# Kernel optimization log

Measured on AMD Instinct MI355X. Metric: run time of the kernel, lower is better.

The kernel has to match this reference:

```python
import jax, jax.numpy as jnp
import numpy as np

P, M, N, H, B, E, K = 50, 512, 1024, 256, 8, 400, 5
ALPHA_MAX, TAU_MAX, RHO_MAX, ETA_MAX = 0.01, 1.0, 1.0, 1.0
LEAK = 0.01  # F.leaky_relu default slope


def _lrelu(x):
    return jnp.where(x >= 0, x, LEAK * x)


def _layernorm(x, g, b, eps=1e-5):
    mu = jnp.mean(x, axis=-1, keepdims=True)
    var = jnp.mean((x - mu) ** 2, axis=-1, keepdims=True)
    return (x - mu) * jax.lax.rsqrt(var + eps) * g + b


def setup_inputs() -> dict:
    ks = iter(jax.random.split(jax.random.key(0), 16))

    def w(fin, fout):
        return jax.random.normal(next(ks), (fin, fout), jnp.float32) * np.float32(np.sqrt(2.0 / (fin + fout)))

    H4 = 4 * H
    inp = {
        'A': jax.random.normal(next(ks), (1, P, M, N), jnp.float32) * 0.05,
        'b': jax.random.normal(next(ks), (B, P, M, 1), jnp.float32),
        'W1': w(2 * N, H), 'b1': jnp.zeros(H), 'bn1_s': jnp.ones(H), 'bn1_t': jnp.zeros(H),
        'W2': w(H, 2 * H), 'b2': jnp.zeros(2 * H), 'bn2_s': jnp.ones(2 * H), 'bn2_t': jnp.zeros(2 * H),
        'W3': w(2 * H, H4), 'b3': jnp.zeros(H4), 'bn3_s': jnp.ones(H4), 'bn3_t': jnp.zeros(H4),
        'W4': w(H4, H4), 'b4': jnp.zeros(H4), 'bn4_s': jnp.ones(H4), 'bn4_t': jnp.zeros(H4),
        'W5': w(H4, H4), 'b5': jnp.zeros(H4), 'bn5_s': jnp.ones(H4), 'bn5_t': jnp.zeros(H4),
        'ln_g': jnp.ones(H4), 'ln_b': jnp.zeros(H4),
        'Wd1': w(P * H4, H4), 'bd1': jnp.zeros(H4), 'lnd1_g': jnp.ones(H4), 'lnd1_b': jnp.zeros(H4),
        'Wd2': w(H4, 2 * H), 'bd2': jnp.zeros(2 * H), 'lnd2_g': jnp.ones(2 * H), 'lnd2_b': jnp.zeros(2 * H),
        'Wd3': w(2 * H, H), 'bd3': jnp.zeros(H), 'lnd3_g': jnp.ones(H), 'lnd3_b': jnp.zeros(H),
        'Wfc': w(H, 4) * 0.1, 'bfc': jnp.zeros(4),
        'edge_index': jax.random.randint(next(ks), (2, E), 0, P),
    }
    return inp


def reference(A, b, W1, b1, bn1_s, bn1_t, W2, b2, bn2_s, bn2_t, W3, b3, bn3_s, bn3_t,
              W4, b4, bn4_s, bn4_t, W5, b5, bn5_s, bn5_t, ln_g, ln_b,
              Wd1, bd1, lnd1_g, lnd1_b, Wd2, bd2, lnd2_g, lnd2_b, Wd3, bd3, lnd3_g, lnd3_b,
              Wfc, bfc, edge_index):
    A0 = A[0]                                             # [P,M,N]
    AtA = jnp.einsum('pmi,pmj->pij', A0, A0)              # [P,N,N]  (compute_Atx(A))
    Atb = jnp.einsum('pmn,bpm->bpn', A0, b[..., 0])[..., None]  # [B,P,N,1]

    src, dst = edge_index[0], edge_index[1]
    ones_e = jnp.ones((E,), A.dtype)
    # sum_neighbors: out-degree of each node p, shape broadcastable to [B,P,1,1]
    sum_nb = jax.ops.segment_sum(ones_e, src, num_segments=P)[None, :, None, None]

    # GCNConv normalization with self loops: norm_ij = deg_i^-1/2 * deg_j^-1/2
    sl = jnp.arange(P)
    src_a = jnp.concatenate([src, sl])
    dst_a = jnp.concatenate([dst, sl])
    deg = jax.ops.segment_sum(jnp.ones((E + P,), A.dtype), dst_a, num_segments=P)
    dinv = jax.lax.rsqrt(deg)
    coef = (dinv[src_a] * dinv[dst_a])[:, None]           # [E+P,1]

    convs = [(W1, b1, bn1_s, bn1_t), (W2, b2, bn2_s, bn2_t), (W3, b3, bn3_s, bn3_t),
             (W4, b4, bn4_s, bn4_t), (W5, b5, bn5_s, bn5_t)]

    def gconv(x, W, bias):                                # x: [P,Cin]
        xw = x @ W
        return jax.ops.segment_sum(xw[src_a] * coef, dst_a, num_segments=P) + bias

    def encode_one(feat):                                 # feat: [P,2N]
        x = feat
        for (W, bias, s, t) in convs:
            # leaky_relu -> BatchNorm1d (eval: affine scale/shift) -> dropout (eval: id)
            x = _lrelu(gconv(x, W, bias)) * s + t
        return _layernorm(x, ln_g, ln_b).reshape(-1)      # [P*4H]

    enc = jax.vmap(encode_one)

    y = jnp.zeros((B, P, N, 1), A.dtype)
    U = jnp.zeros_like(y)
    delta = jnp.zeros_like(y)
    Ys = []
    for k in range(K):
        AtAy = jnp.einsum('pij,bpj->bpi', AtA, y[..., 0])[..., None]  # [B,P,N,1]
        feat = jnp.concatenate([AtAy, Atb], axis=2)[..., 0]           # [B,P,2N]
        code = enc(feat)                                              # [B,P*4H]
        h = _lrelu(_layernorm(code @ Wd1 + bd1, lnd1_g, lnd1_b))
        h = _lrelu(_layernorm(h @ Wd2 + bd2, lnd2_g, lnd2_b))
        h = _lrelu(_layernorm(h @ Wd3 + bd3, lnd3_g, lnd3_b))
        hyp = jnp.clip(jax.nn.sigmoid(h @ Wfc + bfc), 1e-4, 0.99).reshape(B, 4, 1, 1, 1)
        alpha = hyp[:, 0] * ALPHA_MAX
        tau = hyp[:, 1] * TAU_MAX
        rho = hyp[:, 2] * RHO_MAX
        eta = hyp[:, 3] * ETA_MAX
        g = AtAy - Atb + jnp.sign(y) * tau + U * sum_nb + delta * rho
        mg = max(30.0, 100.0 - k)
        g = jnp.clip(g, -mg, mg)
        mv = max(10.0, 200.0 - k * 3)
        y = jnp.clip(y - alpha * g, -mv, mv)
        # compute_delta: for each directed edge (s,d): delta[s]+= (y_s-y_d); delta[d]-= (y_s-y_d)
        diff = y[:, src] - y[:, dst]                                  # [B,E,N,1]
        delta = jnp.zeros_like(y).at[:, src].add(diff).at[:, dst].add(-diff)
        U = jnp.clip(U + delta * eta, -mv, mv)
        Ys.append(y)
    return jnp.stack(Ys)                                              # [K,B,P,N,1]
```

## Files before the change

### kernel.cpp

```cpp
#include <hip/hip_runtime.h>

#define PP 50
#define MM 512
#define NN 1024

constexpr size_t F_ATB   = 0;
constexpr size_t F_ATAY  = F_ATB   + 409600;
constexpr size_t F_Y     = F_ATAY  + 409600;
constexpr size_t F_U     = F_Y     + 409600;
constexpr size_t F_DELTA = F_U     + 409600;
constexpr size_t F_BT    = F_DELTA + 409600;
constexpr size_t F_AYT   = F_BT    + 204800;
constexpr size_t F_Z     = F_AYT   + 204800;
constexpr size_t F_X0    = F_Z     + 917504;
constexpr size_t F_X1    = F_X0    + 409600;
constexpr size_t F_CODET = F_X1    + 409600;
constexpr size_t F_PART  = F_CODET + 409600;
constexpr size_t F_DPART = F_PART  + 3670016;
constexpr size_t F_DPART2= F_DPART + 2097152;
constexpr size_t F_H1    = F_DPART2+ 32768;
constexpr size_t F_H2    = F_H1    + 8192;
constexpr size_t F_H3    = F_H2    + 4096;
constexpr size_t F_HYP   = F_H3    + 2048;
constexpr size_t F_GCCO  = F_HYP   + 64;
constexpr size_t F_SUMNB = F_GCCO  + 512;
constexpr size_t F_END   = F_SUMNB + 64;

__device__ __forceinline__ float lrelu(float v) { return v >= 0.f ? v : 0.01f * v; }

__device__ __forceinline__ void bred2(float& s1, float& s2, float* sm) {
  #pragma unroll
  for (int off = 32; off > 0; off >>= 1) {
    s1 += __shfl_down(s1, off);
    s2 += __shfl_down(s2, off);
  }
  int w = threadIdx.x >> 6, l = threadIdx.x & 63;
  if (l == 0) { sm[w] = s1; sm[4 + w] = s2; }
  __syncthreads();
  s1 = sm[0] + sm[1] + sm[2] + sm[3];
  s2 = sm[4] + sm[5] + sm[6] + sm[7];
}

__global__ __launch_bounds__(512) void ksetup(const int* __restrict__ ei, float* sumnb,
                                              float* gccoef, int* gcoff, int* gcsrc,
                                              int* nbroff, int* nbridx) {
  __shared__ int cin[PP];
  __shared__ int cou[PP];
  __shared__ float sdinv[PP];
  __shared__ int goff[PP + 1], noff[PP + 1];
  int t = threadIdx.x;
  const int* src = ei;
  const int* dst = ei + 400;
  if (t < PP) { cin[t] = 0; cou[t] = 0; }
  __syncthreads();
  if (t < 400) {
    atomicAdd(&cou[src[t]], 1);
    atomicAdd(&cin[dst[t]], 1);
  }
  __syncthreads();
  if (t < PP) {
    sdinv[t] = rsqrtf((float)(cin[t] + 1));
    sumnb[t] = (float)cou[t];
  }
  __syncthreads();
  if (t == 0) {
    goff[0] = 0; noff[0] = 0;
    for (int p = 0; p < PP; ++p) {
      goff[p + 1] = goff[p] + cin[p] + 1;
      noff[p + 1] = noff[p] + cin[p] + cou[p];
    }
  }
  __syncthreads();
  if (t <= PP) { gcoff[t] = goff[t]; nbroff[t] = noff[t]; }
  if (t < 400) {
    int d = dst[t], s = src[t];
    int slot = 0;
    for (int e = 0; e < t; ++e) slot += (dst[e] == d) ? 1 : 0;
    int pos = goff[d] + slot;
    gcsrc[pos] = s;
    gccoef[pos] = sdinv[s] * sdinv[d];
  }
  if (t < PP) {
    int pos = goff[t] + cin[t];
    gcsrc[pos] = t;
    gccoef[pos] = sdinv[t] * sdinv[t];
  }
  if (t < 400) {
    int s = src[t], d = dst[t];
    int so = 0, si = 0;
    for (int e = 0; e < t; ++e) {
      so += (src[e] == s) ? 1 : 0;
      si += (dst[e] == d) ? 1 : 0;
    }
    nbridx[noff[s] + so] = d;
    nbridx[noff[d] + cou[d] + si] = s;
  }
}

__global__ __launch_bounds__(256) void kbt(const float* __restrict__ b, float* __restrict__ bt) {
  int i = blockIdx.x * 256 + threadIdx.x;
  int bb = i / (PP * MM);
  int r = i - bb * (PP * MM);
  bt[r * 8 + bb] = b[i];
}

__global__ __launch_bounds__(256) void katz(const float* __restrict__ A, const float* __restrict__ q,
                                            float* __restrict__ outv) {
  __shared__ float red[4][64][8];
  int nb = blockIdx.x, p = blockIdx.y, t = threadIdx.x;
  int ln = t & 63, mg = t >> 6;
  int n = nb * 64 + ln;
  float acc[8] = {0, 0, 0, 0, 0, 0, 0, 0};
  const float* ap = A + ((size_t)p * MM + mg * 128) * NN + n;
  const float* qp = q + ((size_t)p * MM + mg * 128) * 8;
  for (int m0 = 0; m0 < 128; m0 += 8) {
    float av[8];
    #pragma unroll
    for (int u = 0; u < 8; ++u) av[u] = ap[(size_t)(m0 + u) * NN];
    #pragma unroll
    for (int u = 0; u < 8; ++u) {
      #pragma unroll
      for (int bb = 0; bb < 8; ++bb) acc[bb] += av[u] * qp[(m0 + u) * 8 + bb];
    }
  }
  #pragma unroll
  for (int bb = 0; bb < 8; ++bb) red[mg][ln][bb] = acc[bb];
  __syncthreads();
  if (mg == 0) {
    #pragma unroll
    for (int bb = 0; bb < 8; ++bb) {
      float v = red[0][ln][bb] + red[1][ln][bb] + red[2][ln][bb] + red[3][ln][bb];
      outv[((size_t)bb * PP + p) * NN + n] = v;
    }
  }
}

__global__ __launch_bounds__(256) void kay(const float* __restrict__ A, const float* __restrict__ y,
                                           float* __restrict__ ayt) {
  __shared__ __align__(16) float sy[8][NN];
  int p = blockIdx.x, mb = blockIdx.y, t = threadIdx.x;
  #pragma unroll
  for (int bb = 0; bb < 8; ++bb)
    for (int n = t; n < NN; n += 256) sy[bb][n] = y[(bb * PP + p) * NN + n];
  __syncthreads();
  int w = t >> 6, l = t & 63;
  int mbase = mb * 64 + w * 16;
  for (int i = 0; i < 8; ++i) {
    int m0 = mbase + 2 * i, m1 = m0 + 1;
    float acc0[8] = {0, 0, 0, 0, 0, 0, 0, 0};
    float acc1[8] = {0, 0, 0, 0, 0, 0, 0, 0};
    const float* a0p = A + ((size_t)p * MM + m0) * NN;
    const float* a1p = a0p + NN;
    #pragma unroll
    for (int jj = 0; jj < 4; ++jj) {
      int n0 = 4 * l + 256 * jj;
      float4 a0 = *(const float4*)(a0p + n0);
      float4 a1 = *(const float4*)(a1p + n0);
      #pragma unroll
      for (int bb = 0; bb < 8; ++bb) {
        float4 yv = *(const float4*)&sy[bb][n0];
        acc0[bb] += a0.x * yv.x + a0.y * yv.y + a0.z * yv.z + a0.w * yv.w;
        acc1[bb] += a1.x * yv.x + a1.y * yv.y + a1.z * yv.z + a1.w * yv.w;
      }
    }
    #pragma unroll
    for (int off = 32; off > 0; off >>= 1) {
      #pragma unroll
      for (int bb = 0; bb < 8; ++bb) {
        acc0[bb] += __shfl_down(acc0[bb], off);
        acc1[bb] += __shfl_down(acc1[bb], off);
      }
    }
    if (l == 0) {
      #pragma unroll
      for (int bb = 0; bb < 8; ++bb) {
        ayt[((size_t)p * MM + m0) * 8 + bb] = acc0[bb];
        ayt[((size_t)p * MM + m1) * 8 + bb] = acc1[bb];
      }
    }
  }
}

__global__ __launch_bounds__(256) void kgather1(const float* __restrict__ atay,
                                                const float* __restrict__ atb,
                                                float* __restrict__ z,
                                                const int* __restrict__ gcoff,
                                                const int* __restrict__ gcsrc,
                                                const float* __restrict__ gccoef, int first) {
  int r = blockIdx.x, cc = blockIdx.y, t = threadIdx.x;
  size_t zi = (size_t)r * 2048 + (size_t)cc * 256 + t;
  if (r >= 400) { z[zi] = 0.f; return; }
  int srcA = (cc < 4) ? 1 : 0;
  if (srcA && first) { z[zi] = 0.f; return; }
  int b = r / 50, p = r - b * 50;
  int c = (srcA ? cc * 256 : (cc - 4) * 256) + t;
  const float* src = srcA ? atay : atb;
  float acc = 0.f;
  int o0 = gcoff[p], o1 = gcoff[p + 1];
  for (int idx = o0; idx < o1; ++idx)
    acc += gccoef[idx] * src[((size_t)b * 50 + gcsrc[idx]) * 1024 + c];
  z[zi] = acc;
}

__global__ __launch_bounds__(256) void kgatherX(const float* __restrict__ x, float* __restrict__ z,
                                                int Cin, const int* __restrict__ gcoff,
                                                const int* __restrict__ gcsrc,
                                                const float* __restrict__ gccoef) {
  int r = blockIdx.x, cc = blockIdx.y, t = threadIdx.x;
  int c = cc * 256 + t;
  size_t zi = (size_t)r * Cin + c;
  if (r >= 400) { z[zi] = 0.f; return; }
  int b = r / 50, p = r - b * 50;
  float acc = 0.f;
  int o0 = gcoff[p], o1 = gcoff[p + 1];
  for (int idx = o0; idx < o1; ++idx)
    acc += gccoef[idx] * x[((size_t)b * 50 + gcsrc[idx]) * Cin + c];
  z[zi] = acc;
}

__global__ __launch_bounds__(256) void kgemm(const float* __restrict__ X, const float* __restrict__ W,
                                             float* __restrict__ part, int K, int C, int krange) {
  int cb = blockIdx.x, rb = blockIdx.y, s = blockIdx.z;
  int t = threadIdx.x;
  __shared__ __align__(16) float As[16][64];
  __shared__ __align__(16) float Bs[16][68];
  int rbase = rb * 64, cbase = cb * 64;
  int k0 = s * krange, kend = k0 + krange;
  float acc[4][4] = {};
  int tx = t & 15, ty = t >> 4;
  int lrow = t >> 2, lk = (t & 3) * 4;
  int brow = t >> 4, bc = (t & 15) * 4;
  for (int k = k0; k < kend; k += 16) {
    float4 av = *(const float4*)(X + (size_t)(rbase + lrow) * K + k + lk);
    As[lk + 0][lrow] = av.x;
    As[lk + 1][lrow] = av.y;
    As[lk + 2][lrow] = av.z;
    As[lk + 3][lrow] = av.w;
    *(float4*)&Bs[brow][bc] = *(const float4*)(W + (size_t)(k + brow) * C + cbase + bc);
    __syncthreads();
    #pragma unroll
    for (int kk = 0; kk < 16; ++kk) {
      float4 a = *(const float4*)&As[kk][ty * 4];
      float4 b = *(const float4*)&Bs[kk][tx * 4];
      float aa[4] = {a.x, a.y, a.z, a.w};
      float bb[4] = {b.x, b.y, b.z, b.w};
      #pragma unroll
      for (int i = 0; i < 4; ++i)
        #pragma unroll
        for (int j = 0; j < 4; ++j) acc[i][j] += aa[i] * bb[j];
    }
    __syncthreads();
  }
  #pragma unroll
  for (int i = 0; i < 4; ++i) {
    int r = rbase + ty * 4 + i;
    *(float4*)&part[((size_t)s * 448 + r) * C + cbase + tx * 4] =
        make_float4(acc[i][0], acc[i][1], acc[i][2], acc[i][3]);
  }
}

template <int NCH, bool LASTLN>
__global__ __launch_bounds__(256) void kredE(const float* __restrict__ part, int S,
                                             const float* __restrict__ bias,
                                             const float* __restrict__ bns,
                                             const float* __restrict__ bnt,
                                             float* __restrict__ xout,
                                             const float* __restrict__ lng,
                                             const float* __restrict__ lnb,
                                             float* __restrict__ codet) {
  __shared__ float smr[8];
  constexpr int C = NCH * 256;
  int r = blockIdx.x, t = threadIdx.x;
  float vals[NCH];
  #pragma unroll
  for (int ch = 0; ch < NCH; ++ch) {
    int c = ch * 256 + t;
    float acc = 0.f;
    const float* pp = part + (size_t)r * C + c;
    #pragma unroll 4
    for (int s = 0; s < S; ++s) acc += pp[(size_t)s * 448 * C];
    float v = lrelu(acc + bias[c]);
    vals[ch] = v * bns[c] + bnt[c];
  }
  if (!LASTLN) {
    #pragma unroll
    for (int ch = 0; ch < NCH; ++ch)
      xout[(size_t)r * C + ch * 256 + t] = vals[ch];
  } else {
    float s1 = 0.f, s2 = 0.f;
    #pragma unroll
    for (int ch = 0; ch < NCH; ++ch) { s1 += vals[ch]; s2 += vals[ch] * vals[ch]; }
    bred2(s1, s2, smr);
    float mu = s1 / (float)C;
    float var = s2 / (float)C - mu * mu;
    float rs = rsqrtf(var + 1e-5f);
    int b = r / 50, p = r - b * 50;
    #pragma unroll
    for (int ch = 0; ch < NCH; ++ch) {
      int c = ch * 256 + t;
      codet[((size_t)p * C + c) * 8 + b] = (vals[ch] - mu) * rs * lng[c] + lnb[c];
    }
  }
}

__global__ __launch_bounds__(256) void kwd1(const float* __restrict__ W,
                                            const float* __restrict__ in_t,
                                            float* __restrict__ dpart) {
  int t = threadIdx.x, s = blockIdx.x;
  int k0 = s * 200;
  float4 acc[8];
  #pragma unroll
  for (int b = 0; b < 8; ++b) acc[b] = make_float4(0.f, 0.f, 0.f, 0.f);
  const float* wp = W + (size_t)k0 * 1024 + 4 * t;
  const float* qp = in_t + (size_t)k0 * 8;
  for (int k = 0; k < 200; k += 4) {
    float4 wv[4], qa[4], qb[4];
    #pragma unroll
    for (int u = 0; u < 4; ++u) {
      wv[u] = *(const float4*)(wp + (size_t)(k + u) * 1024);
      qa[u] = *(const float4*)(qp + (k + u) * 8);
      qb[u] = *(const float4*)(qp + (k + u) * 8 + 4);
    }
    #pragma unroll
    for (int u = 0; u < 4; ++u) {
      float qs[8] = {qa[u].x, qa[u].y, qa[u].z, qa[u].w, qb[u].x, qb[u].y, qb[u].z, qb[u].w};
      #pragma unroll
      for (int b = 0; b < 8; ++b) {
        acc[b].x += wv[u].x * qs[b];
        acc[b].y += wv[u].y * qs[b];
        acc[b].z += wv[u].z * qs[b];
        acc[b].w += wv[u].w * qs[b];
      }
    }
  }
  #pragma unroll
  for (int b = 0; b < 8; ++b)
    *(float4*)&dpart[(size_t)(s * 8 + b) * 1024 + 4 * t] = acc[b];
}

__global__ __launch_bounds__(256) void kredA(const float* __restrict__ dpart,
                                             float* __restrict__ dpart2) {
  int cb = blockIdx.x, sg = blockIdx.y, b = blockIdx.z, t = threadIdx.x;
  int c = cb * 256 + t;
  float acc = 0.f;
  const float* pp = dpart + ((size_t)(sg * 64) * 8 + b) * 1024 + c;
  #pragma unroll 8
  for (int i = 0; i < 64; ++i) acc += pp[(size_t)i * 8 * 1024];
  dpart2[((size_t)sg * 8 + b) * 1024 + c] = acc;
}

__global__ __launch_bounds__(128) void kwdS(const float* __restrict__ W,
                                            const float* __restrict__ in_t,
                                            float* __restrict__ part, int C, int krange) {
  int t = threadIdx.x, s = blockIdx.x;
  int k0 = s * krange;
  float4 acc[8];
  #pragma unroll
  for (int b = 0; b < 8; ++b) acc[b] = make_float4(0.f, 0.f, 0.f, 0.f);
  const float* wp = W + (size_t)k0 * C + 4 * t;
  const float* qp = in_t + (size_t)k0 * 8;
  for (int k = 0; k < krange; ++k) {
    float4 wv = *(const float4*)(wp + (size_t)k * C);
    float4 qa = *(const float4*)(qp + k * 8);
    float4 qb = *(const float4*)(qp + k * 8 + 4);
    float qs[8] = {qa.x, qa.y, qa.z, qa.w, qb.x, qb.y, qb.z, qb.w};
    #pragma unroll
    for (int b = 0; b < 8; ++b) {
      acc[b].x += wv.x * qs[b];
      acc[b].y += wv.y * qs[b];
      acc[b].z += wv.z * qs[b];
      acc[b].w += wv.w * qs[b];
    }
  }
  #pragma unroll
  for (int b = 0; b < 8; ++b)
    *(float4*)&part[(size_t)(s * 8 + b) * C + 4 * t] = acc[b];
}

__global__ __launch_bounds__(1024) void kred(const float* __restrict__ part, int S, int C,
                                             const float* __restrict__ bias,
                                             const float* __restrict__ g,
                                             const float* __restrict__ be,
                                             float* __restrict__ out_t) {
  __shared__ float sm[32];
  int b = blockIdx.x, t = threadIdx.x;
  float v = bias[t];
  const float* pp = part + (size_t)b * C + t;
  #pragma unroll 4
  for (int s = 0; s < S; ++s) v += pp[(size_t)s * 8 * C];
  float s1 = v, s2 = v * v;
  #pragma unroll
  for (int off = 32; off > 0; off >>= 1) {
    s1 += __shfl_down(s1, off);
    s2 += __shfl_down(s2, off);
  }
  int w = t >> 6, l = t & 63;
  int nw = blockDim.x >> 6;
  if (l == 0) { sm[w] = s1; sm[16 + w] = s2; }
  __syncthreads();
  s1 = 0.f; s2 = 0.f;
  for (int i = 0; i < nw; ++i) { s1 += sm[i]; s2 += sm[16 + i]; }
  float inv = 1.f / (float)C;
  float mu = s1 * inv;
  float var = s2 * inv - mu * mu;
  float rs = rsqrtf(var + 1e-5f);
  float o = lrelu((v - mu) * rs * g[t] + be[t]);
  out_t[t * 8 + b] = o;
}

__global__ __launch_bounds__(256) void kwfc(const float* __restrict__ Wfc, const float* __restrict__ bfc,
                                            const float* __restrict__ h3t, float* __restrict__ hyp) {
  __shared__ float sd[32][257];
  int t = threadIdx.x;
  float4 w = *(const float4*)(Wfc + t * 4);
  #pragma unroll
  for (int bb = 0; bb < 8; ++bb) {
    float x = h3t[t * 8 + bb];
    sd[bb * 4 + 0][t] = x * w.x;
    sd[bb * 4 + 1][t] = x * w.y;
    sd[bb * 4 + 2][t] = x * w.z;
    sd[bb * 4 + 3][t] = x * w.w;
  }
  __syncthreads();
  if (t < 32) {
    float s = 0.f;
    for (int i = 0; i < 256; ++i) s += sd[t][i];
    s += bfc[t & 3];
    float sig = 1.f / (1.f + expf(-s));
    sig = fminf(fmaxf(sig, 1e-4f), 0.99f);
    hyp[t] = sig;
  }
}

__global__ __launch_bounds__(256) void kyupd(const float* __restrict__ atay, const float* __restrict__ atb,
                                             float* y, const float* __restrict__ U,
                                             const float* __restrict__ delta,
                                             const float* __restrict__ hyp,
                                             const float* __restrict__ sumnb, float* __restrict__ outp,
                                             float mg, float mv, int first) {
  int i = blockIdx.x * 256 + threadIdx.x;
  int bb = i / (PP * NN);
  int rem = i - bb * (PP * NN);
  int p = rem >> 10;
  float alpha = hyp[bb * 4 + 0] * 0.01f;
  float g;
  float yv;
  if (first) {
    yv = 0.f;
    g = -atb[i];
  } else {
    float tau = hyp[bb * 4 + 1];
    float rho = hyp[bb * 4 + 2];
    yv = y[i];
    float sg = (yv > 0.f) ? 1.f : ((yv < 0.f) ? -1.f : 0.f);
    g = atay[i] - atb[i] + sg * tau + U[i] * sumnb[p] + delta[i] * rho;
  }
  g = fminf(fmaxf(g, -mg), mg);
  float yn = yv - alpha * g;
  yn = fminf(fmaxf(yn, -mv), mv);
  y[i] = yn;
  outp[i] = yn;
}

__global__ __launch_bounds__(256) void kdeltaU(const float* __restrict__ y, float* __restrict__ delta,
                                               float* __restrict__ U, const float* __restrict__ hyp,
                                               const int* __restrict__ nbroff,
                                               const int* __restrict__ nbridx, float mv, int first) {
  int t = threadIdx.x;
  int n = blockIdx.x * 256 + t;
  int p = blockIdx.y;
  int bb = blockIdx.z;
  int o0 = nbroff[p], o1 = nbroff[p + 1];
  int base = bb * (PP * NN) + p * NN;
  float d = (float)(o1 - o0) * y[base + n];
  for (int idx = o0; idx < o1; ++idx) {
    int q = nbridx[idx];
    d -= y[bb * (PP * NN) + q * NN + n];
  }
  delta[base + n] = d;
  float eta = hyp[bb * 4 + 3];
  float u0 = first ? 0.f : U[base + n];
  float u = u0 + d * eta;
  U[base + n] = fminf(fmaxf(u, -mv), mv);
}

extern "C" void kernel_launch(void* const* d_in, const int* in_sizes, int n_in,
                              void* d_out, int out_size, void* d_ws, size_t ws_size,
                              hipStream_t stream) {
  const float* A    = (const float*)d_in[0];
  const float* bvec = (const float*)d_in[1];
  const float* W1 = (const float*)d_in[2];
  const float* b1 = (const float*)d_in[3];
  const float* bn1s = (const float*)d_in[4];
  const float* bn1t = (const float*)d_in[5];
  const float* W2 = (const float*)d_in[6];
  const float* b2 = (const float*)d_in[7];
  const float* bn2s = (const float*)d_in[8];
  const float* bn2t = (const float*)d_in[9];
  const float* W3 = (const float*)d_in[10];
  const float* b3 = (const float*)d_in[11];
  const float* bn3s = (const float*)d_in[12];
  const float* bn3t = (const float*)d_in[13];
  const float* W4 = (const float*)d_in[14];
  const float* b4 = (const float*)d_in[15];
  const float* bn4s = (const float*)d_in[16];
  const float* bn4t = (const float*)d_in[17];
  const float* W5 = (const float*)d_in[18];
  const float* b5 = (const float*)d_in[19];
  const float* bn5s = (const float*)d_in[20];
  const float* bn5t = (const float*)d_in[21];
  const float* lng = (const float*)d_in[22];
  const float* lnb = (const float*)d_in[23];
  const float* Wd1 = (const float*)d_in[24];
  const float* bd1 = (const float*)d_in[25];
  const float* lnd1g = (const float*)d_in[26];
  const float* lnd1b = (const float*)d_in[27];
  const float* Wd2 = (const float*)d_in[28];
  const float* bd2 = (const float*)d_in[29];
  const float* lnd2g = (const float*)d_in[30];
  const float* lnd2b = (const float*)d_in[31];
  const float* Wd3 = (const float*)d_in[32];
  const float* bd3 = (const float*)d_in[33];
  const float* lnd3g = (const float*)d_in[34];
  const float* lnd3b = (const float*)d_in[35];
  const float* Wfc = (const float*)d_in[36];
  const float* bfc = (const float*)d_in[37];
  const int* ei = (const int*)d_in[38];

  float* out = (float*)d_out;
  float* wsf = (float*)d_ws;
  float* atb = wsf + F_ATB;
  float* atay = wsf + F_ATAY;
  float* yb = wsf + F_Y;
  float* Ub = wsf + F_U;
  float* db = wsf + F_DELTA;
  float* bt = wsf + F_BT;
  float* ayt = wsf + F_AYT;
  float* z = wsf + F_Z;
  float* x0 = wsf + F_X0;
  float* x1 = wsf + F_X1;
  float* codet = wsf + F_CODET;
  float* part = wsf + F_PART;
  float* dpart = wsf + F_DPART;
  float* dpart2 = wsf + F_DPART2;
  float* h1t = wsf + F_H1;
  float* h2t = wsf + F_H2;
  float* h3t = wsf + F_H3;
  float* hyp = wsf + F_HYP;
  float* gccoef = wsf + F_GCCO;
  float* sumnb = wsf + F_SUMNB;
  int* wsi = (int*)(wsf + F_END);
  int* gcoff = wsi;
  int* gcsrc = wsi + 64;
  int* nbroff = wsi + 576;
  int* nbridx = wsi + 640;

  ksetup<<<1, 512, 0, stream>>>(ei, sumnb, gccoef, gcoff, gcsrc, nbroff, nbridx);
  kbt<<<800, 256, 0, stream>>>(bvec, bt);
  katz<<<dim3(16, 50), 256, 0, stream>>>(A, bt, atb);

  const float mgs[5] = {100.f, 99.f, 98.f, 97.f, 96.f};
  const float mvs[5] = {200.f, 197.f, 194.f, 191.f, 188.f};

  for (int k = 0; k < 5; ++k) {
    if (k > 0) {
      kay<<<dim3(50, 8), 256, 0, stream>>>(A, yb, ayt);
      katz<<<dim3(16, 50), 256, 0, stream>>>(A, ayt, atay);
    }
    kgather1<<<dim3(448, 8), 256, 0, stream>>>(atay, atb, z, gcoff, gcsrc, gccoef, k == 0);
    kgemm<<<dim3(4, 7, 16), 256, 0, stream>>>(z, W1, part, 2048, 256, 128);
    kredE<1, false><<<400, 256, 0, stream>>>(part, 16, b1, bn1s, bn1t, x0, nullptr, nullptr, nullptr);
    kgatherX<<<dim3(448, 1), 256, 0, stream>>>(x0, z, 256, gcoff, gcsrc, gccoef);
    kgemm<<<dim3(8, 7, 8), 256, 0, stream>>>(z, W2, part, 256, 512, 32);
    kredE<2, false><<<400, 256, 0, stream>>>(part, 8, b2, bn2s, bn2t, x1, nullptr, nullptr, nullptr);
    kgatherX<<<dim3(448, 2), 256, 0, stream>>>(x1, z, 512, gcoff, gcsrc, gccoef);
    kgemm<<<dim3(16, 7, 8), 256, 0, stream>>>(z, W3, part, 512, 1024, 64);
    kredE<4, false><<<400, 256, 0, stream>>>(part, 8, b3, bn3s, bn3t, x0, nullptr, nullptr, nullptr);
    kgatherX<<<dim3(448, 4), 256, 0, stream>>>(x0, z, 1024, gcoff, gcsrc, gccoef);
    kgemm<<<dim3(16, 7, 8), 256, 0, stream>>>(z, W4, part, 1024, 1024, 128);
    kredE<4, false><<<400, 256, 0, stream>>>(part, 8, b4, bn4s, bn4t, x1, nullptr, nullptr, nullptr);
    kgatherX<<<dim3(448, 4), 256, 0, stream>>>(x1, z, 1024, gcoff, gcsrc, gccoef);
    kgemm<<<dim3(16, 7, 8), 256, 0, stream>>>(z, W5, part, 1024, 1024, 128);
    kredE<4, true><<<400, 256, 0, stream>>>(part, 8, b5, bn5s, bn5t, nullptr, lng, lnb, codet);
    kwd1<<<256, 256, 0, stream>>>(Wd1, codet, dpart);
    kredA<<<dim3(4, 4, 8), 256, 0, stream>>>(dpart, dpart2);
    kred<<<8, 1024, 0, stream>>>(dpart2, 4, 1024, bd1, lnd1g, lnd1b, h1t);
    kwdS<<<64, 128, 0, stream>>>(Wd2, h1t, dpart, 512, 16);
    kred<<<8, 512, 0, stream>>>(dpart, 64, 512, bd2, lnd2g, lnd2b, h2t);
    kwdS<<<32, 64, 0, stream>>>(Wd3, h2t, dpart, 256, 16);
    kred<<<8, 256, 0, stream>>>(dpart, 32, 256, bd3, lnd3g, lnd3b, h3t);
    kwfc<<<1, 256, 0, stream>>>(Wfc, bfc, h3t, hyp);
    kyupd<<<1600, 256, 0, stream>>>(atay, atb, yb, Ub, db, hyp, sumnb,
                                    out + (size_t)k * 409600, mgs[k], mvs[k], k == 0);
    kdeltaU<<<dim3(4, 50, 8), 256, 0, stream>>>(yb, db, Ub, hyp, nbroff, nbridx, mvs[k], k == 0);
  }
}
```

Measured before the change: 1.568 ms.

## Hoist Atb gather, skip zero half of first GEMM, fuse y/delta/U update, retile kay

The graph-conv gather of Atb now runs once before the loop, and a new split-input GEMM reads Atay and Atb halves from separate buffers. At k==0 it computes only the Atb half, because the Atay half is zero then. The y update and the delta/U update are fused into one kernel that keeps the new y slice in shared memory for neighbour differences. kay is retiled so each lane handles one batch and a 128-column chunk over 4 rows, and kwd1 gets twice the split count with the partial buffers aliased. The fused update kernel launches only 128 blocks, which may leave the GPU underused.

```diff
diff --git a/kernel.cpp b/kernel.cpp
--- a/kernel.cpp
+++ b/kernel.cpp
@@ -12,12 +12,12 @@
 constexpr size_t F_BT    = F_DELTA + 409600;
 constexpr size_t F_AYT   = F_BT    + 204800;
 constexpr size_t F_Z     = F_AYT   + 204800;
-constexpr size_t F_X0    = F_Z     + 917504;
+constexpr size_t F_ZB    = F_Z     + 458752;
+constexpr size_t F_X0    = F_ZB    + 458752;
 constexpr size_t F_X1    = F_X0    + 409600;
 constexpr size_t F_CODET = F_X1    + 409600;
 constexpr size_t F_PART  = F_CODET + 409600;
-constexpr size_t F_DPART = F_PART  + 3670016;
-constexpr size_t F_DPART2= F_DPART + 2097152;
+constexpr size_t F_DPART2= F_PART  + 4194304;
 constexpr size_t F_H1    = F_DPART2+ 32768;
 constexpr size_t F_H2    = F_H1    + 8192;
 constexpr size_t F_H3    = F_H2    + 4096;
@@ -139,67 +139,39 @@
                                            float* __restrict__ ayt) {
   __shared__ __align__(16) float sy[8][NN];
   int p = blockIdx.x, mb = blockIdx.y, t = threadIdx.x;
-  #pragma unroll
-  for (int bb = 0; bb < 8; ++bb)
-    for (int n = t; n < NN; n += 256) sy[bb][n] = y[(bb * PP + p) * NN + n];
+  for (int idx = t; idx < 8 * NN; idx += 256) {
+    int bb = idx >> 10, n = idx & 1023;
+    sy[bb][n] = y[((size_t)bb * PP + p) * NN + n];
+  }
   __syncthreads();
   int w = t >> 6, l = t & 63;
-  int mbase = mb * 64 + w * 16;
-  for (int i = 0; i < 8; ++i) {
-    int m0 = mbase + 2 * i, m1 = m0 + 1;
-    float acc0[8] = {0, 0, 0, 0, 0, 0, 0, 0};
-    float acc1[8] = {0, 0, 0, 0, 0, 0, 0, 0};
-    const float* a0p = A + ((size_t)p * MM + m0) * NN;
-    const float* a1p = a0p + NN;
-    #pragma unroll
-    for (int jj = 0; jj < 4; ++jj) {
-      int n0 = 4 * l + 256 * jj;
-      float4 a0 = *(const float4*)(a0p + n0);
-      float4 a1 = *(const float4*)(a1p + n0);
+  int b = l & 7, nc = l >> 3;
+  int n0 = nc * 128;
+  for (int i = 0; i < 4; ++i) {
+    int m0 = mb * 64 + w * 16 + i * 4;
+    float acc[4] = {0.f, 0.f, 0.f, 0.f};
+    const float* ap = A + ((size_t)p * MM + m0) * NN + n0;
+    #pragma unroll 8
+    for (int j = 0; j < 32; ++j) {
+      float4 yv = *(const float4*)&sy[b][n0 + 4 * j];
       #pragma unroll
-      for (int bb = 0; bb < 8; ++bb) {
-        float4 yv = *(const float4*)&sy[bb][n0];
-        acc0[bb] += a0.x * yv.x + a0.y * yv.y + a0.z * yv.z + a0.w * yv.w;
-        acc1[bb] += a1.x * yv.x + a1.y * yv.y + a1.z * yv.z + a1.w * yv.w;
+      for (int mm = 0; mm < 4; ++mm) {
+        float4 av = *(const float4*)(ap + (size_t)mm * NN + 4 * j);
+        acc[mm] += av.x * yv.x + av.y * yv.y + av.z * yv.z + av.w * yv.w;
       }
     }
     #pragma unroll
-    for (int off = 32; off > 0; off >>= 1) {
+    for (int mm = 0; mm < 4; ++mm) {
+      acc[mm] += __shfl_xor(acc[mm], 8);
+      acc[mm] += __shfl_xor(acc[mm], 16);
+      acc[mm] += __shfl_xor(acc[mm], 32);
+    }
+    if (nc == 0) {
       #pragma unroll
-      for (int bb = 0; bb < 8; ++bb) {
-        acc0[bb] += __shfl_down(acc0[bb], off);
-        acc1[bb] += __shfl_down(acc1[bb], off);
-      }
-    }
-    if (l == 0) {
-      #pragma unroll
-      for (int bb = 0; bb < 8; ++bb) {
-        ayt[((size_t)p * MM + m0) * 8 + bb] = acc0[bb];
-        ayt[((size_t)p * MM + m1) * 8 + bb] = acc1[bb];
-      }
-    }
-  }
-}
-
-__global__ __launch_bounds__(256) void kgather1(const float* __restrict__ atay,
-                                                const float* __restrict__ atb,
-                                                float* __restrict__ z,
-                                                const int* __restrict__ gcoff,
-                                                const int* __restrict__ gcsrc,
-                                                const float* __restrict__ gccoef, int first) {
-  int r = blockIdx.x, cc = blockIdx.y, t = threadIdx.x;
-  size_t zi = (size_t)r * 2048 + (size_t)cc * 256 + t;
-  if (r >= 400) { z[zi] = 0.f; return; }
-  int srcA = (cc < 4) ? 1 : 0;
-  if (srcA && first) { z[zi] = 0.f; return; }
-  int b = r / 50, p = r - b * 50;
-  int c = (srcA ? cc * 256 : (cc - 4) * 256) + t;
-  const float* src = srcA ? atay : atb;
-  float acc = 0.f;
-  int o0 = gcoff[p], o1 = gcoff[p + 1];
-  for (int idx = o0; idx < o1; ++idx)
-    acc += gccoef[idx] * src[((size_t)b * 50 + gcsrc[idx]) * 1024 + c];
-  z[zi] = acc;
+      for (int mm = 0; mm < 4; ++mm)
+        ayt[(size_t)((size_t)p * MM + m0 + mm) * 8 + b] = acc[mm];
+    }
+  }
 }
 
 __global__ __launch_bounds__(256) void kgatherX(const float* __restrict__ x, float* __restrict__ z,
@@ -259,6 +231,51 @@
   }
 }
 
+__global__ __launch_bounds__(256) void kgemmC(const float* __restrict__ XA, const float* __restrict__ XB,
+                                              const float* __restrict__ W, float* __restrict__ part,
+                                              int C, int krange, int koff) {
+  int cb = blockIdx.x, rb = blockIdx.y, s = blockIdx.z;
+  int t = threadIdx.x;
+  __shared__ __align__(16) float As[16][64];
+  __shared__ __align__(16) float Bs[16][68];
+  int rbase = rb * 64, cbase = cb * 64;
+  int k0 = koff + s * krange, kend = k0 + krange;
+  float acc[4][4] = {};
+  int tx = t & 15, ty = t >> 4;
+  int lrow = t >> 2, lk = (t & 3) * 4;
+  int brow = t >> 4, bc = (t & 15) * 4;
+  for (int k = k0; k < kend; k += 16) {
+    int r = rbase + lrow;
+    const float* xp = (k < 1024) ? (XA + (size_t)r * 1024 + k)
+                                 : (XB + (size_t)r * 1024 + (k - 1024));
+    float4 av = *(const float4*)(xp + lk);
+    As[lk + 0][lrow] = av.x;
+    As[lk + 1][lrow] = av.y;
+    As[lk + 2][lrow] = av.z;
+    As[lk + 3][lrow] = av.w;
+    *(float4*)&Bs[brow][bc] = *(const float4*)(W + (size_t)(k + brow) * C + cbase + bc);
+    __syncthreads();
+    #pragma unroll
+    for (int kk = 0; kk < 16; ++kk) {
+      float4 a = *(const float4*)&As[kk][ty * 4];
+      float4 b = *(const float4*)&Bs[kk][tx * 4];
+      float aa[4] = {a.x, a.y, a.z, a.w};
+      float bb[4] = {b.x, b.y, b.z, b.w};
+      #pragma unroll
+      for (int i = 0; i < 4; ++i)
+        #pragma unroll
+        for (int j = 0; j < 4; ++j) acc[i][j] += aa[i] * bb[j];
+    }
+    __syncthreads();
+  }
+  #pragma unroll
+  for (int i = 0; i < 4; ++i) {
+    int r = rbase + ty * 4 + i;
+    *(float4*)&part[((size_t)s * 448 + r) * C + cbase + tx * 4] =
+        make_float4(acc[i][0], acc[i][1], acc[i][2], acc[i][3]);
+  }
+}
+
 template <int NCH, bool LASTLN>
 __global__ __launch_bounds__(256) void kredE(const float* __restrict__ part, int S,
                                              const float* __restrict__ bias,
@@ -307,22 +324,22 @@
                                             const float* __restrict__ in_t,
                                             float* __restrict__ dpart) {
   int t = threadIdx.x, s = blockIdx.x;
-  int k0 = s * 200;
+  int k0 = s * 100;
   float4 acc[8];
   #pragma unroll
   for (int b = 0; b < 8; ++b) acc[b] = make_float4(0.f, 0.f, 0.f, 0.f);
   const float* wp = W + (size_t)k0 * 1024 + 4 * t;
   const float* qp = in_t + (size_t)k0 * 8;
-  for (int k = 0; k < 200; k += 4) {
-    float4 wv[4], qa[4], qb[4];
-    #pragma unroll
-    for (int u = 0; u < 4; ++u) {
+  for (int k = 0; k < 100; k += 5) {
+    float4 wv[5], qa[5], qb[5];
+    #pragma unroll
+    for (int u = 0; u < 5; ++u) {
       wv[u] = *(const float4*)(wp + (size_t)(k + u) * 1024);
       qa[u] = *(const float4*)(qp + (k + u) * 8);
       qb[u] = *(const float4*)(qp + (k + u) * 8 + 4);
     }
     #pragma unroll
-    for (int u = 0; u < 4; ++u) {
+    for (int u = 0; u < 5; ++u) {
       float qs[8] = {qa[u].x, qa[u].y, qa[u].z, qa[u].w, qb[u].x, qb[u].y, qb[u].z, qb[u].w};
       #pragma unroll
       for (int b = 0; b < 8; ++b) {
@@ -343,9 +360,9 @@
   int cb = blockIdx.x, sg = blockIdx.y, b = blockIdx.z, t = threadIdx.x;
   int c = cb * 256 + t;
   float acc = 0.f;
-  const float* pp = dpart + ((size_t)(sg * 64) * 8 + b) * 1024 + c;
+  const float* pp = dpart + ((size_t)(sg * 128) * 8 + b) * 1024 + c;
   #pragma unroll 8
-  for (int i = 0; i < 64; ++i) acc += pp[(size_t)i * 8 * 1024];
+  for (int i = 0; i < 128; ++i) acc += pp[(size_t)i * 8 * 1024];
   dpart2[((size_t)sg * 8 + b) * 1024 + c] = acc;
 }
 
@@ -386,7 +403,7 @@
   int b = blockIdx.x, t = threadIdx.x;
   float v = bias[t];
   const float* pp = part + (size_t)b * C + t;
-  #pragma unroll 4
+  #pragma unroll 8
   for (int s = 0; s < S; ++s) v += pp[(size_t)s * 8 * C];
   float s1 = v, s2 = v * v;
   #pragma unroll
@@ -432,56 +449,54 @@
   }
 }
 
-__global__ __launch_bounds__(256) void kyupd(const float* __restrict__ atay, const float* __restrict__ atb,
-                                             float* y, const float* __restrict__ U,
-                                             const float* __restrict__ delta,
+__global__ __launch_bounds__(256) void kiter(const float* __restrict__ atay,
+                                             const float* __restrict__ atb,
+                                             float* __restrict__ y, float* __restrict__ U,
+                                             float* __restrict__ delta,
                                              const float* __restrict__ hyp,
-                                             const float* __restrict__ sumnb, float* __restrict__ outp,
+                                             const float* __restrict__ sumnb,
+                                             float* __restrict__ outp,
+                                             const int* __restrict__ nbroff,
+                                             const int* __restrict__ nbridx,
                                              float mg, float mv, int first) {
-  int i = blockIdx.x * 256 + threadIdx.x;
-  int bb = i / (PP * NN);
-  int rem = i - bb * (PP * NN);
-  int p = rem >> 10;
-  float alpha = hyp[bb * 4 + 0] * 0.01f;
-  float g;
-  float yv;
-  if (first) {
-    yv = 0.f;
-    g = -atb[i];
-  } else {
-    float tau = hyp[bb * 4 + 1];
-    float rho = hyp[bb * 4 + 2];
-    yv = y[i];
-    float sg = (yv > 0.f) ? 1.f : ((yv < 0.f) ? -1.f : 0.f);
-    g = atay[i] - atb[i] + sg * tau + U[i] * sumnb[p] + delta[i] * rho;
-  }
-  g = fminf(fmaxf(g, -mg), mg);
-  float yn = yv - alpha * g;
-  yn = fminf(fmaxf(yn, -mv), mv);
-  y[i] = yn;
-  outp[i] = yn;
-}
-
-__global__ __launch_bounds__(256) void kdeltaU(const float* __restrict__ y, float* __restrict__ delta,
-                                               float* __restrict__ U, const float* __restrict__ hyp,
-                                               const int* __restrict__ nbroff,
-                                               const int* __restrict__ nbridx, float mv, int first) {
-  int t = threadIdx.x;
-  int n = blockIdx.x * 256 + t;
-  int p = blockIdx.y;
-  int bb = blockIdx.z;
-  int o0 = nbroff[p], o1 = nbroff[p + 1];
-  int base = bb * (PP * NN) + p * NN;
-  float d = (float)(o1 - o0) * y[base + n];
-  for (int idx = o0; idx < o1; ++idx) {
-    int q = nbridx[idx];
-    d -= y[bb * (PP * NN) + q * NN + n];
-  }
-  delta[base + n] = d;
-  float eta = hyp[bb * 4 + 3];
-  float u0 = first ? 0.f : U[base + n];
-  float u = u0 + d * eta;
-  U[base + n] = fminf(fmaxf(u, -mv), mv);
+  __shared__ float ynew[3200];
+  int nc = blockIdx.x, b = blockIdx.y, t = threadIdx.x;
+  float alpha = hyp[b * 4 + 0] * 0.01f;
+  float tau = hyp[b * 4 + 1];
+  float rho = hyp[b * 4 + 2];
+  float eta = hyp[b * 4 + 3];
+  int nbase = nc * 64;
+  for (int idx = t; idx < 3200; idx += 256) {
+    int p = idx >> 6, n = nbase + (idx & 63);
+    size_t gi = ((size_t)b * PP + p) * NN + n;
+    float g, yv;
+    if (first) {
+      yv = 0.f;
+      g = -atb[gi];
+    } else {
+      yv = y[gi];
+      float sg = (yv > 0.f) ? 1.f : ((yv < 0.f) ? -1.f : 0.f);
+      g = atay[gi] - atb[gi] + sg * tau + U[gi] * sumnb[p] + delta[gi] * rho;
+    }
+    g = fminf(fmaxf(g, -mg), mg);
+    float yn = yv - alpha * g;
+    yn = fminf(fmaxf(yn, -mv), mv);
+    y[gi] = yn;
+    outp[gi] = yn;
+    ynew[idx] = yn;
+  }
+  __syncthreads();
+  for (int idx = t; idx < 3200; idx += 256) {
+    int p = idx >> 6, n6 = idx & 63;
+    size_t gi = ((size_t)b * PP + p) * NN + nbase + n6;
+    int o0 = nbroff[p], o1 = nbroff[p + 1];
+    float d = (float)(o1 - o0) * ynew[idx];
+    for (int j = o0; j < o1; ++j) d -= ynew[(nbridx[j] << 6) + n6];
+    delta[gi] = d;
+    float u0 = first ? 0.f : U[gi];
+    float u = u0 + d * eta;
+    U[gi] = fminf(fmaxf(u, -mv), mv);
+  }
 }
 
 extern "C" void kernel_launch(void* const* d_in, const int* in_sizes, int n_in,
@@ -536,12 +551,13 @@
   float* db = wsf + F_DELTA;
   float* bt = wsf + F_BT;
   float* ayt = wsf + F_AYT;
-  float* z = wsf + F_Z;
+  float* zA = wsf + F_Z;
+  float* zB = wsf + F_ZB;
   float* x0 = wsf + F_X0;
   float* x1 = wsf + F_X1;
   float* codet = wsf + F_CODET;
   float* part = wsf + F_PART;
-  float* dpart = wsf + F_DPART;
+  float* dpart = part;
   float* dpart2 = wsf + F_DPART2;
   float* h1t = wsf + F_H1;
   float* h2t = wsf + F_H2;
@@ -558,6 +574,7 @@
   ksetup<<<1, 512, 0, stream>>>(ei, sumnb, gccoef, gcoff, gcsrc, nbroff, nbridx);
   kbt<<<800, 256, 0, stream>>>(bvec, bt);
   katz<<<dim3(16, 50), 256, 0, stream>>>(A, bt, atb);
+  kgatherX<<<dim3(448, 4), 256, 0, stream>>>(atb, zB, 1024, gcoff, gcsrc, gccoef);
 
   const float mgs[5] = {100.f, 99.f, 98.f, 97.f, 96.f};
   const float mvs[5] = {200.f, 197.f, 194.f, 191.f, 188.f};
@@ -567,22 +584,27 @@
       kay<<<dim3(50, 8), 256, 0, stream>>>(A, yb, ayt);
       katz<<<dim3(16, 50), 256, 0, stream>>>(A, ayt, atay);
     }
-    kgather1<<<dim3(448, 8), 256, 0, stream>>>(atay, atb, z, gcoff, gcsrc, gccoef, k == 0);
-    kgemm<<<dim3(4, 7, 16), 256, 0, stream>>>(z, W1, part, 2048, 256, 128);
-    kredE<1, false><<<400, 256, 0, stream>>>(part, 16, b1, bn1s, bn1t, x0, nullptr, nullptr, nullptr);
-    kgatherX<<<dim3(448, 1), 256, 0, stream>>>(x0, z, 256, gcoff, gcsrc, gccoef);
-    kgemm<<<dim3(8, 7, 8), 256, 0, stream>>>(z, W2, part, 256, 512, 32);
+    if (k == 0) {
+      kgemmC<<<dim3(4, 7, 4), 256, 0, stream>>>(zA, zB, W1, part, 256, 256, 1024);
+      kredE<1, false><<<400, 256, 0, stream>>>(part, 4, b1, bn1s, bn1t, x0, nullptr, nullptr, nullptr);
+    } else {
+      kgatherX<<<dim3(448, 4), 256, 0, stream>>>(atay, zA, 1024, gcoff, gcsrc, gccoef);
+      kgemmC<<<dim3(4, 7, 8), 256, 0, stream>>>(zA, zB, W1, part, 256, 256, 0);
+      kredE<1, false><<<400, 256, 0, stream>>>(part, 8, b1, bn1s, bn1t, x0, nullptr, nullptr, nullptr);
+    }
+    kgatherX<<<dim3(448, 1), 256, 0, stream>>>(x0, zA, 256, gcoff, gcsrc, gccoef);
+    kgemm<<<dim3(8, 7, 8), 256, 0, stream>>>(zA, W2, part, 256, 512, 32);
     kredE<2, false><<<400, 256, 0, stream>>>(part, 8, b2, bn2s, bn2t, x1, nullptr, nullptr, nullptr);
-    kgatherX<<<dim3(448, 2), 256, 0, stream>>>(x1, z, 512, gcoff, gcsrc, gccoef);
-    kgemm<<<dim3(16, 7, 8), 256, 0, stream>>>(z, W3, part, 512, 1024, 64);
+    kgatherX<<<dim3(448, 2), 256, 0, stream>>>(x1, zA, 512, gcoff, gcsrc, gccoef);
+    kgemm<<<dim3(16, 7, 8), 256, 0, stream>>>(zA, W3, part, 512, 1024, 64);
     kredE<4, false><<<400, 256, 0, stream>>>(part, 8, b3, bn3s, bn3t, x0, nullptr, nullptr, nullptr);
-    kgatherX<<<dim3(448, 4), 256, 0, stream>>>(x0, z, 1024, gcoff, gcsrc, gccoef);
-    kgemm<<<dim3(16, 7, 8), 256, 0, stream>>>(z, W4, part, 1024, 1024, 128);
+    kgatherX<<<dim3(448, 4), 256, 0, stream>>>(x0, zA, 1024, gcoff, gcsrc, gccoef);
+    kgemm<<<dim3(16, 7, 8), 256, 0, stream>>>(zA, W4, part, 1024, 1024, 128);
     kredE<4, false><<<400, 256, 0, stream>>>(part, 8, b4, bn4s, bn4t, x1, nullptr, nullptr, nullptr);
-    kgatherX<<<dim3(448, 4), 256, 0, stream>>>(x1, z, 1024, gcoff, gcsrc, gccoef);
-    kgemm<<<dim3(16, 7, 8), 256, 0, stream>>>(z, W5, part, 1024, 1024, 128);
+    kgatherX<<<dim3(448, 4), 256, 0, stream>>>(x1, zA, 1024, gcoff, gcsrc, gccoef);
+    kgemm<<<dim3(16, 7, 8), 256, 0, stream>>>(zA, W5, part, 1024, 1024, 128);
     kredE<4, true><<<400, 256, 0, stream>>>(part, 8, b5, bn5s, bn5t, nullptr, lng, lnb, codet);
-    kwd1<<<256, 256, 0, stream>>>(Wd1, codet, dpart);
+    kwd1<<<512, 256, 0, stream>>>(Wd1, codet, dpart);
     kredA<<<dim3(4, 4, 8), 256, 0, stream>>>(dpart, dpart2);
     kred<<<8, 1024, 0, stream>>>(dpart2, 4, 1024, bd1, lnd1g, lnd1b, h1t);
     kwdS<<<64, 128, 0, stream>>>(Wd2, h1t, dpart, 512, 16);
@@ -590,8 +612,8 @@
     kwdS<<<32, 64, 0, stream>>>(Wd3, h2t, dpart, 256, 16);
     kred<<<8, 256, 0, stream>>>(dpart, 32, 256, bd3, lnd3g, lnd3b, h3t);
     kwfc<<<1, 256, 0, stream>>>(Wfc, bfc, h3t, hyp);
-    kyupd<<<1600, 256, 0, stream>>>(atay, atb, yb, Ub, db, hyp, sumnb,
-                                    out + (size_t)k * 409600, mgs[k], mvs[k], k == 0);
-    kdeltaU<<<dim3(4, 50, 8), 256, 0, stream>>>(yb, db, Ub, hyp, nbroff, nbridx, mvs[k], k == 0);
-  }
-}
+    kiter<<<dim3(16, 8), 256, 0, stream>>>(atay, atb, yb, Ub, db, hyp, sumnb,
+                                           out + (size_t)k * 409600, nbroff, nbridx,
+                                           mgs[k], mvs[k], k == 0);
+  }
+}
```

Result: slower. 1.751 ms (+11.7%).
